# Performance work log

Hardware: AMD Instinct MI355X
Metric: run time of the kernel (lower is better)

The kernel has to match this reference:

```python
import jax, jax.numpy as jnp
import numpy as np

H = 64  # rnn_size == input_size
CANVAS = 25


def _init_params(key, vocab_size):
    ks = jax.random.split(key, 14)
    s = 0.05
    p = {}
    p['embed'] = jax.random.normal(ks[0], (vocab_size + 1, H), jnp.float32) * s
    p['W_ih'] = jax.random.normal(ks[1], (4 * H, H), jnp.float32) * s
    p['W_hh'] = jax.random.normal(ks[2], (4 * H, H), jnp.float32) * s
    p['b_ih'] = jax.random.normal(ks[3], (4 * H,), jnp.float32) * s
    p['b_hh'] = jax.random.normal(ks[4], (4 * H,), jnp.float32) * s
    p['Wc'] = jax.random.normal(ks[5], (3, H), jnp.float32) * s
    p['bc'] = jax.random.normal(ks[6], (3,), jnp.float32) * s
    p['Ws'] = jax.random.normal(ks[7], (3, H), jnp.float32) * s
    p['bs'] = jax.random.normal(ks[8], (3,), jnp.float32) * s
    p['Wo'] = jax.random.normal(ks[9], (2, H), jnp.float32) * s
    p['bo'] = jax.random.normal(ks[10], (2,), jnp.float32) * s
    p['Wr1'] = jax.random.normal(ks[11], (32, H + 1 + 4), jnp.float32) * s
    p['br1'] = jnp.zeros((32,), jnp.float32)
    p['Wr2'] = jax.random.normal(ks[12], (1, 32), jnp.float32) * s
    p['br2'] = jnp.zeros((1,), jnp.float32)
    return p


def setup_inputs() -> dict:
    key = jax.random.key(0)
    k1, k2, k3, k4, k5 = jax.random.split(key, 5)
    B, T, V = 4096, 128, 32000
    inp = {
        'inst': jax.random.randint(k1, (B, T), 0, V, dtype=jnp.int64)
        if jax.config.jax_enable_x64 else jax.random.randint(k1, (B, T), 0, V, dtype=jnp.int32),
        'prev_canvas': jax.random.normal(k2, (B, CANVAS, 4), jnp.float32),
        'ref_obj': jax.random.normal(k3, (B, 4), jnp.float32),
        'target_obj': jax.random.normal(k4, (B, 4), jnp.float32),
    }
    inp.update(_init_params(k5, V))
    return inp


def _encode(inst, embed, W_ih, W_hh, b_ih, b_hh):
    # inst: [B, T] -> h: [B, H] via sequential LSTMCell
    xs = embed[inst]                       # [B, T, H]
    xs = jnp.swapaxes(xs, 0, 1)            # [T, B, H]
    B = inst.shape[0]
    h0 = jnp.zeros((B, H), xs.dtype)
    c0 = jnp.zeros((B, H), xs.dtype)

    def step(carry, x):
        h, c = carry
        gates = x @ W_ih.T + b_ih + h @ W_hh.T + b_hh   # [B, 4H]
        i, f, g, o = jnp.split(gates, 4, axis=-1)
        i, f, o = jax.nn.sigmoid(i), jax.nn.sigmoid(f), jax.nn.sigmoid(o)
        c = f * c + i * jnp.tanh(g)
        h = o * jnp.tanh(c)
        return (h, c), None

    (h, _), _ = jax.lax.scan(step, (h0, c0), xs)
    return h


def _act_tag(inst):
    # 1.0 if last token with value >= 1 equals 9, else 0.0
    T = inst.shape[1]
    mask = inst >= 1                                   # [B, T]
    last_pos = T - 1 - jnp.argmax(mask[:, ::-1], axis=1)
    last_val = jnp.take_along_axis(inst, last_pos[:, None], axis=1)[:, 0]
    tag = jnp.where((last_val == 9) & mask.any(axis=1), 1.0, 0.0)
    return tag.astype(jnp.float32)


def reference(inst, prev_canvas, ref_obj, target_obj, embed, W_ih, W_hh, b_ih, b_hh,
              Wc, bc, Ws, bs, Wo, bo, Wr1, br1, Wr2, br2):
    h = _encode(inst, embed, W_ih, W_hh, b_ih, b_hh)           # [B, H]
    tag = _act_tag(inst)                                       # [B]
    inst2 = jnp.concatenate([h, tag[:, None]], axis=1)         # [B, H+1]
    inst2 = jnp.broadcast_to(inst2[:, None, :], (h.shape[0], CANVAS, H + 1))
    feat = jnp.concatenate([inst2, prev_canvas], axis=2)       # [B, 25, 69]
    hid = jax.nn.relu(jnp.einsum('bnf,of->bno', feat, Wr1) + br1)
    score = (jnp.einsum('bno,ro->bnr', hid, Wr2) + br2)[..., 0]  # [B, 25]
    weight = jax.nn.softmax(score, axis=1)
    ref_pred = jnp.einsum('bn,bnd->bd', weight, prev_canvas)   # [B, 4]
    offset = jnp.clip(h @ Wo.T + bo, -1.0, 1.0)                # hardtanh, [B, 2]
    color_out = jax.nn.log_softmax(h @ Wc.T + bc, axis=1)      # [B, 3]
    shape_out = jax.nn.log_softmax(h @ Ws.T + bs, axis=1)      # [B, 3]
    row_out = ref_pred[:, 2] + offset[:, 0]
    col_out = ref_pred[:, 3] + offset[:, 1]
    return (color_out, shape_out, row_out, col_out)
```

## Files before the change

kernel.cpp:

```cpp
#include <hip/hip_runtime.h>
#include <hip/hip_bf16.h>

#define HH 64
#define TT 128
#define BT 16

typedef __attribute__((ext_vector_type(8))) short bf16x8;
typedef __attribute__((ext_vector_type(4))) float f32x4;

__device__ __forceinline__ unsigned short f2bf(float f) {
  union { float f; unsigned u; } v; v.f = f;
  return (unsigned short)((v.u + 0x7FFFu + ((v.u >> 16) & 1u)) >> 16);
}
__device__ __forceinline__ float sigm(float x) {
  return __builtin_amdgcn_rcpf(1.f + __builtin_amdgcn_exp2f(-1.44269504f * x));
}
__device__ __forceinline__ float tanh_(float x) {
  x = fminf(fmaxf(x, -15.f), 15.f);
  float e = __builtin_amdgcn_exp2f(2.88539008f * x);
  return (e - 1.f) * __builtin_amdgcn_rcpf(e + 1.f);
}
__device__ __forceinline__ float wred64(float v) {
#pragma unroll
  for (int s = 32; s; s >>= 1) v += __shfl_xor(v, s);
  return v;
}

__global__ void convert_embed(const float* __restrict__ src,
                              unsigned short* __restrict__ dst, int n) {
  int base = (blockIdx.x * 256 + threadIdx.x) * 4;
  if (base + 4 <= n) {
    float4 v = *(const float4*)(src + base);
    ushort4 r;
    r.x = f2bf(v.x); r.y = f2bf(v.y); r.z = f2bf(v.z); r.w = f2bf(v.w);
    *(ushort4*)(dst + base) = r;
  } else {
    for (int k = base; k < n; k++) dst[k] = f2bf(src[k]);
  }
}

#define MFMA(acc, a, b) acc = __builtin_amdgcn_mfma_f32_16x16x32_bf16(a, b, acc, 0, 0, 0)

__global__ __launch_bounds__(256, 1) void lstm_k(
    const int* __restrict__ inst, const unsigned short* __restrict__ ebf,
    const float* __restrict__ Wih, const float* __restrict__ Whh,
    const float* __restrict__ bih, const float* __restrict__ bhh,
    float* __restrict__ hbuf)
{
  __shared__ int tokT[TT * BT];
  __shared__ unsigned short hsh[2 * BT * HH];

  const int tid  = threadIdx.x;
  const int lane = tid & 63;
  const int w    = tid >> 6;
  const int fr   = lane & 15;
  const int fg   = lane >> 4;
  const int b0   = blockIdx.x * BT;
  const int jcol = w * 16 + fr;

  for (int i = tid; i < BT * TT; i += 256)
    tokT[(i & (TT - 1)) * BT + (i >> 7)] = inst[b0 * TT + i];
  for (int i = tid; i < BT * HH; i += 256) hsh[i] = 0;

  bf16x8 wih[4][2], whh[4][2];
  float bias[4];
#pragma unroll
  for (int q = 0; q < 4; q++) {
    const int n = (w + q * 4) * 16 + fr;
    bias[q] = bih[n] + bhh[n];
#pragma unroll
    for (int kt = 0; kt < 2; kt++) {
      const float* pa = Wih + n * 64 + kt * 32 + fg * 8;
      const float* pb = Whh + n * 64 + kt * 32 + fg * 8;
      bf16x8 fa, fb;
#pragma unroll
      for (int j = 0; j < 8; j++) { fa[j] = (short)f2bf(pa[j]); fb[j] = (short)f2bf(pb[j]); }
      wih[q][kt] = fa; whh[q][kt] = fb;
    }
  }

  __syncthreads();

  bf16x8 xa0, xa1;
  {
    const int tk = tokT[0 * BT + fr];
    const unsigned short* p = ebf + tk * 64 + fg * 8;
    xa0 = *(const bf16x8*)p;
    xa1 = *(const bf16x8*)(p + 32);
  }

  float cst[4] = {0.f, 0.f, 0.f, 0.f};
  float hkeep[4] = {0.f, 0.f, 0.f, 0.f};

  for (int t = 0; t < TT; t++) {
    bf16x8 xn0 = xa0, xn1 = xa1;
    if (t + 1 < TT) {
      const int tk = tokT[(t + 1) * BT + fr];
      const unsigned short* p = ebf + tk * 64 + fg * 8;
      xn0 = *(const bf16x8*)p;
      xn1 = *(const bf16x8*)(p + 32);
    }

    const char* hb = (const char*)hsh + (t & 1) * (BT * HH * 2);
    const int sx = (fr & 7) << 4;
    bf16x8 ha0 = *(const bf16x8*)(hb + ((fr * 128 + fg * 16) ^ sx));
    bf16x8 ha1 = *(const bf16x8*)(hb + ((fr * 128 + 64 + fg * 16) ^ sx));

    f32x4 D0 = {0.f,0.f,0.f,0.f}, D1 = {0.f,0.f,0.f,0.f},
          D2 = {0.f,0.f,0.f,0.f}, D3 = {0.f,0.f,0.f,0.f};
    MFMA(D0, xa0, wih[0][0]); MFMA(D0, xa1, wih[0][1]);
    MFMA(D1, xa0, wih[1][0]); MFMA(D1, xa1, wih[1][1]);
    MFMA(D2, xa0, wih[2][0]); MFMA(D2, xa1, wih[2][1]);
    MFMA(D3, xa0, wih[3][0]); MFMA(D3, xa1, wih[3][1]);
    MFMA(D0, ha0, whh[0][0]); MFMA(D0, ha1, whh[0][1]);
    MFMA(D1, ha0, whh[1][0]); MFMA(D1, ha1, whh[1][1]);
    MFMA(D2, ha0, whh[2][0]); MFMA(D2, ha1, whh[2][1]);
    MFMA(D3, ha0, whh[3][0]); MFMA(D3, ha1, whh[3][1]);

    char* hwb = (char*)hsh + ((t + 1) & 1) * (BT * HH * 2);
#pragma unroll
    for (int r = 0; r < 4; r++) {
      const float gi = sigm(D0[r] + bias[0]);
      const float gf = sigm(D1[r] + bias[1]);
      const float gg = tanh_(D2[r] + bias[2]);
      const float go = sigm(D3[r] + bias[3]);
      const float cn = gf * cst[r] + gi * gg;
      cst[r] = cn;
      const float hn = go * tanh_(cn);
      hkeep[r] = hn;
      const int m = fg * 4 + r;
      *(unsigned short*)(hwb + ((m * 128 + 2 * jcol) ^ ((m & 7) << 4))) = f2bf(hn);
    }
    __syncthreads();
    xa0 = xn0; xa1 = xn1;
  }

#pragma unroll
  for (int r = 0; r < 4; r++) {
    const int m = fg * 4 + r;
    hbuf[(size_t)(b0 + m) * 64 + jcol] = hkeep[r];
  }
}

__global__ __launch_bounds__(256, 2) void head_k(
    const int* __restrict__ inst, const float* __restrict__ canvas,
    const float* __restrict__ hbuf,
    const float* __restrict__ Wc, const float* __restrict__ bc,
    const float* __restrict__ Ws, const float* __restrict__ bs,
    const float* __restrict__ Wo, const float* __restrict__ bo,
    const float* __restrict__ Wr1, const float* __restrict__ br1,
    const float* __restrict__ Wr2, const float* __restrict__ br2,
    float* __restrict__ out, int B)
{
  __shared__ float Wr1_s[32 * 69];
  __shared__ float h_s[4][64];
  __shared__ float cv_s[4][100];
  __shared__ float sc_s[4][25];

  const int tid = threadIdx.x, lane = tid & 63, w = tid >> 6;
  const int b = blockIdx.x * 4 + w;

  for (int i = tid; i < 32 * 69; i += 256) Wr1_s[i] = Wr1[i];
  const float hj = hbuf[(size_t)b * 64 + lane];
  h_s[w][lane] = hj;
  for (int idx = lane; idx < 100; idx += 64) cv_s[w][idx] = canvas[(size_t)b * 100 + idx];

  const int t1 = inst[(size_t)b * TT + lane];
  const int t2 = inst[(size_t)b * TT + 64 + lane];
  int key = -1;
  if (t1 >= 1) key = (lane << 16) | t1;
  if (t2 >= 1) key = ((64 + lane) << 16) | t2;
#pragma unroll
  for (int s = 32; s; s >>= 1) key = max(key, __shfl_xor(key, s));
  const float tag = (key >= 0 && (key & 0xFFFF) == 9) ? 1.f : 0.f;

  __syncthreads();

  const int o = lane & 31, half = lane >> 5;
  float base = br1[o] + Wr1_s[o * 69 + 64] * tag;
  for (int f = 0; f < 64; f++) base += Wr1_s[o * 69 + f] * h_s[w][f];
  const float wr2o = Wr2[o];
  const int n0 = half ? 13 : 0, n1 = half ? 25 : 13;
  for (int n = n0; n < n1; n++) {
    float acc = base;
#pragma unroll
    for (int d = 0; d < 4; d++) acc += Wr1_s[o * 69 + 65 + d] * cv_s[w][n * 4 + d];
    float p = wr2o * fmaxf(acc, 0.f);
#pragma unroll
    for (int s = 16; s; s >>= 1) p += __shfl_xor(p, s, 32);
    if (o == 0) sc_s[w][n] = p + br2[0];
  }
  __syncthreads();

  float mx = -1e30f;
  for (int n = 0; n < 25; n++) mx = fmaxf(mx, sc_s[w][n]);
  float sum = 0.f, rp2 = 0.f, rp3 = 0.f;
  for (int n = 0; n < 25; n++) {
    float e = __expf(sc_s[w][n] - mx);
    sum += e;
    rp2 += e * cv_s[w][n * 4 + 2];
    rp3 += e * cv_s[w][n * 4 + 3];
  }
  const float inv = 1.f / sum;

  float c0 = wred64(hj * Wc[lane]),      c1 = wred64(hj * Wc[64 + lane]),  c2 = wred64(hj * Wc[128 + lane]);
  float s0 = wred64(hj * Ws[lane]),      s1 = wred64(hj * Ws[64 + lane]),  s2 = wred64(hj * Ws[128 + lane]);
  float o0 = wred64(hj * Wo[lane]),      o1 = wred64(hj * Wo[64 + lane]);
  c0 += bc[0]; c1 += bc[1]; c2 += bc[2];
  s0 += bs[0]; s1 += bs[1]; s2 += bs[2];
  o0 = fminf(fmaxf(o0 + bo[0], -1.f), 1.f);
  o1 = fminf(fmaxf(o1 + bo[1], -1.f), 1.f);

  const float cm = fmaxf(c0, fmaxf(c1, c2));
  const float cl = cm + __logf(__expf(c0 - cm) + __expf(c1 - cm) + __expf(c2 - cm));
  const float smx = fmaxf(s0, fmaxf(s1, s2));
  const float sl = smx + __logf(__expf(s0 - smx) + __expf(s1 - smx) + __expf(s2 - smx));

  if (lane == 0) {
    out[b * 3 + 0] = c0 - cl; out[b * 3 + 1] = c1 - cl; out[b * 3 + 2] = c2 - cl;
    float* shp = out + (size_t)3 * B;
    shp[b * 3 + 0] = s0 - sl; shp[b * 3 + 1] = s1 - sl; shp[b * 3 + 2] = s2 - sl;
    out[(size_t)6 * B + b] = rp2 * inv + o0;
    out[(size_t)7 * B + b] = rp3 * inv + o1;
  }
}

extern "C" void kernel_launch(void* const* d_in, const int* in_sizes, int n_in,
                              void* d_out, int out_size, void* d_ws, size_t ws_size,
                              hipStream_t stream) {
  const int*   inst   = (const int*)  d_in[0];
  const float* canvas = (const float*)d_in[1];
  const float* embed  = (const float*)d_in[4];
  const float* Wih    = (const float*)d_in[5];
  const float* Whh    = (const float*)d_in[6];
  const float* bih    = (const float*)d_in[7];
  const float* bhh    = (const float*)d_in[8];
  const float* Wc     = (const float*)d_in[9];
  const float* bc     = (const float*)d_in[10];
  const float* Ws_    = (const float*)d_in[11];
  const float* bs     = (const float*)d_in[12];
  const float* Wo     = (const float*)d_in[13];
  const float* bo     = (const float*)d_in[14];
  const float* Wr1    = (const float*)d_in[15];
  const float* br1    = (const float*)d_in[16];
  const float* Wr2    = (const float*)d_in[17];
  const float* br2    = (const float*)d_in[18];

  const int B  = in_sizes[0] / TT;
  const int NE = in_sizes[4];

  unsigned short* ebf = (unsigned short*)d_ws;
  size_t ebytes = ((size_t)NE * 2 + 255) / 256 * 256;
  float* hbuf = (float*)((char*)d_ws + ebytes);

  convert_embed<<<(NE / 4 + 255) / 256, 256, 0, stream>>>(embed, ebf, NE);
  lstm_k<<<B / BT, 256, 0, stream>>>(inst, ebf, Wih, Whh, bih, bhh, hbuf);
  head_k<<<B / 4, 256, 0, stream>>>(inst, canvas, hbuf, Wc, bc, Ws_, bs, Wo, bo,
                                    Wr1, br1, Wr2, br2, (float*)d_out, B);
}
```

Measured before the change: 108.6 us.

## Fuse head into LSTM kernel and split gate work across 8 waves

The LSTM kernel now runs 512 threads per block. Half the waves compute the input and cell gates, and the other half compute the forget and output gates plus the cell update, exchanging results through shared memory with two barriers per step. The input projection for the next step is computed off the critical path after the first barrier. The head computation is fused into the same kernel, reading h from shared memory, which removes the hbuf round trip and one kernel launch. The cost is a second barrier per timestep and extra shared-memory traffic in the recurrent loop.

```diff
diff --git a/kernel.cpp b/kernel.cpp
--- a/kernel.cpp
+++ b/kernel.cpp
@@ -12,17 +12,15 @@
   union { float f; unsigned u; } v; v.f = f;
   return (unsigned short)((v.u + 0x7FFFu + ((v.u >> 16) & 1u)) >> 16);
 }
-__device__ __forceinline__ float sigm(float x) {
-  return __builtin_amdgcn_rcpf(1.f + __builtin_amdgcn_exp2f(-1.44269504f * x));
-}
-__device__ __forceinline__ float tanh_(float x) {
-  x = fminf(fmaxf(x, -15.f), 15.f);
-  float e = __builtin_amdgcn_exp2f(2.88539008f * x);
-  return (e - 1.f) * __builtin_amdgcn_rcpf(e + 1.f);
-}
-__device__ __forceinline__ float wred64(float v) {
-#pragma unroll
-  for (int s = 32; s; s >>= 1) v += __shfl_xor(v, s);
+__device__ __forceinline__ float rcp_(float x) { return __builtin_amdgcn_rcpf(x); }
+__device__ __forceinline__ float exp2_(float x) { return __builtin_amdgcn_exp2f(x); }
+
+#define L2E 1.44269504f
+#define L2E2 2.88539008f
+
+__device__ __forceinline__ float red32(float v) {
+#pragma unroll
+  for (int s = 16; s; s >>= 1) v += __shfl_xor(v, s, 32);
   return v;
 }
 
@@ -41,110 +39,11 @@
 
 #define MFMA(acc, a, b) acc = __builtin_amdgcn_mfma_f32_16x16x32_bf16(a, b, acc, 0, 0, 0)
 
-__global__ __launch_bounds__(256, 1) void lstm_k(
+__global__ __launch_bounds__(512, 1) void lstm_k(
     const int* __restrict__ inst, const unsigned short* __restrict__ ebf,
     const float* __restrict__ Wih, const float* __restrict__ Whh,
     const float* __restrict__ bih, const float* __restrict__ bhh,
-    float* __restrict__ hbuf)
-{
-  __shared__ int tokT[TT * BT];
-  __shared__ unsigned short hsh[2 * BT * HH];
-
-  const int tid  = threadIdx.x;
-  const int lane = tid & 63;
-  const int w    = tid >> 6;
-  const int fr   = lane & 15;
-  const int fg   = lane >> 4;
-  const int b0   = blockIdx.x * BT;
-  const int jcol = w * 16 + fr;
-
-  for (int i = tid; i < BT * TT; i += 256)
-    tokT[(i & (TT - 1)) * BT + (i >> 7)] = inst[b0 * TT + i];
-  for (int i = tid; i < BT * HH; i += 256) hsh[i] = 0;
-
-  bf16x8 wih[4][2], whh[4][2];
-  float bias[4];
-#pragma unroll
-  for (int q = 0; q < 4; q++) {
-    const int n = (w + q * 4) * 16 + fr;
-    bias[q] = bih[n] + bhh[n];
-#pragma unroll
-    for (int kt = 0; kt < 2; kt++) {
-      const float* pa = Wih + n * 64 + kt * 32 + fg * 8;
-      const float* pb = Whh + n * 64 + kt * 32 + fg * 8;
-      bf16x8 fa, fb;
-#pragma unroll
-      for (int j = 0; j < 8; j++) { fa[j] = (short)f2bf(pa[j]); fb[j] = (short)f2bf(pb[j]); }
-      wih[q][kt] = fa; whh[q][kt] = fb;
-    }
-  }
-
-  __syncthreads();
-
-  bf16x8 xa0, xa1;
-  {
-    const int tk = tokT[0 * BT + fr];
-    const unsigned short* p = ebf + tk * 64 + fg * 8;
-    xa0 = *(const bf16x8*)p;
-    xa1 = *(const bf16x8*)(p + 32);
-  }
-
-  float cst[4] = {0.f, 0.f, 0.f, 0.f};
-  float hkeep[4] = {0.f, 0.f, 0.f, 0.f};
-
-  for (int t = 0; t < TT; t++) {
-    bf16x8 xn0 = xa0, xn1 = xa1;
-    if (t + 1 < TT) {
-      const int tk = tokT[(t + 1) * BT + fr];
-      const unsigned short* p = ebf + tk * 64 + fg * 8;
-      xn0 = *(const bf16x8*)p;
-      xn1 = *(const bf16x8*)(p + 32);
-    }
-
-    const char* hb = (const char*)hsh + (t & 1) * (BT * HH * 2);
-    const int sx = (fr & 7) << 4;
-    bf16x8 ha0 = *(const bf16x8*)(hb + ((fr * 128 + fg * 16) ^ sx));
-    bf16x8 ha1 = *(const bf16x8*)(hb + ((fr * 128 + 64 + fg * 16) ^ sx));
-
-    f32x4 D0 = {0.f,0.f,0.f,0.f}, D1 = {0.f,0.f,0.f,0.f},
-          D2 = {0.f,0.f,0.f,0.f}, D3 = {0.f,0.f,0.f,0.f};
-    MFMA(D0, xa0, wih[0][0]); MFMA(D0, xa1, wih[0][1]);
-    MFMA(D1, xa0, wih[1][0]); MFMA(D1, xa1, wih[1][1]);
-    MFMA(D2, xa0, wih[2][0]); MFMA(D2, xa1, wih[2][1]);
-    MFMA(D3, xa0, wih[3][0]); MFMA(D3, xa1, wih[3][1]);
-    MFMA(D0, ha0, whh[0][0]); MFMA(D0, ha1, whh[0][1]);
-    MFMA(D1, ha0, whh[1][0]); MFMA(D1, ha1, whh[1][1]);
-    MFMA(D2, ha0, whh[2][0]); MFMA(D2, ha1, whh[2][1]);
-    MFMA(D3, ha0, whh[3][0]); MFMA(D3, ha1, whh[3][1]);
-
-    char* hwb = (char*)hsh + ((t + 1) & 1) * (BT * HH * 2);
-#pragma unroll
-    for (int r = 0; r < 4; r++) {
-      const float gi = sigm(D0[r] + bias[0]);
-      const float gf = sigm(D1[r] + bias[1]);
-      const float gg = tanh_(D2[r] + bias[2]);
-      const float go = sigm(D3[r] + bias[3]);
-      const float cn = gf * cst[r] + gi * gg;
-      cst[r] = cn;
-      const float hn = go * tanh_(cn);
-      hkeep[r] = hn;
-      const int m = fg * 4 + r;
-      *(unsigned short*)(hwb + ((m * 128 + 2 * jcol) ^ ((m & 7) << 4))) = f2bf(hn);
-    }
-    __syncthreads();
-    xa0 = xn0; xa1 = xn1;
-  }
-
-#pragma unroll
-  for (int r = 0; r < 4; r++) {
-    const int m = fg * 4 + r;
-    hbuf[(size_t)(b0 + m) * 64 + jcol] = hkeep[r];
-  }
-}
-
-__global__ __launch_bounds__(256, 2) void head_k(
-    const int* __restrict__ inst, const float* __restrict__ canvas,
-    const float* __restrict__ hbuf,
+    const float* __restrict__ canvas,
     const float* __restrict__ Wc, const float* __restrict__ bc,
     const float* __restrict__ Ws, const float* __restrict__ bs,
     const float* __restrict__ Wo, const float* __restrict__ bo,
@@ -152,76 +51,189 @@
     const float* __restrict__ Wr2, const float* __restrict__ br2,
     float* __restrict__ out, int B)
 {
+  __shared__ int tokT[TT * BT];
+  __shared__ unsigned short hsh[2 * BT * HH];
+  __shared__ float a_s[16][66];
   __shared__ float Wr1_s[32 * 69];
-  __shared__ float h_s[4][64];
-  __shared__ float cv_s[4][100];
-  __shared__ float sc_s[4][25];
-
-  const int tid = threadIdx.x, lane = tid & 63, w = tid >> 6;
-  const int b = blockIdx.x * 4 + w;
-
-  for (int i = tid; i < 32 * 69; i += 256) Wr1_s[i] = Wr1[i];
-  const float hj = hbuf[(size_t)b * 64 + lane];
-  h_s[w][lane] = hj;
-  for (int idx = lane; idx < 100; idx += 64) cv_s[w][idx] = canvas[(size_t)b * 100 + idx];
-
-  const int t1 = inst[(size_t)b * TT + lane];
-  const int t2 = inst[(size_t)b * TT + 64 + lane];
+
+  const int tid  = threadIdx.x;
+  const int lane = tid & 63;
+  const int w    = tid >> 6;
+  const int wid  = w & 3;
+  const int hi   = w >> 2;
+  const int fr   = lane & 15;
+  const int fg   = lane >> 4;
+  const int b0   = blockIdx.x * BT;
+  const int jcol = wid * 16 + fr;
+  const int n0   = hi * 64 + jcol;
+  const int n1   = n0 + 128;
+
+  for (int i = tid; i < BT * TT; i += 512)
+    tokT[(i & (TT - 1)) * BT + (i >> 7)] = inst[b0 * TT + i];
+  for (int i = tid; i < BT * HH; i += 512) hsh[i] = 0;
+  for (int i = tid; i < 32 * 69; i += 512) Wr1_s[i] = Wr1[i];
+
+  bf16x8 wt[2][2][2];
+  float nb0, sb1;
+#pragma unroll
+  for (int tile = 0; tile < 2; tile++) {
+    const int n = tile ? n1 : n0;
+#pragma unroll
+    for (int kt = 0; kt < 2; kt++) {
+      const float* pa = Wih + n * 64 + kt * 32 + fg * 8;
+      const float* pb = Whh + n * 64 + kt * 32 + fg * 8;
+      bf16x8 fa, fb;
+#pragma unroll
+      for (int j = 0; j < 8; j++) { fa[j] = (short)f2bf(pa[j]); fb[j] = (short)f2bf(pb[j]); }
+      wt[tile][kt][0] = fa; wt[tile][kt][1] = fb;
+    }
+  }
+  nb0 = -L2E * (bih[n0] + bhh[n0]);
+  sb1 = (hi ? -L2E : L2E2) * (bih[n1] + bhh[n1]);
+
+  bf16x8 xa0, xa1;
+  {
+    const int tk = tokT[0 * BT + fr];
+    const unsigned short* p = ebf + tk * 64 + fg * 8;
+    xa0 = *(const bf16x8*)p; xa1 = *(const bf16x8*)(p + 32);
+  }
+  f32x4 Dx0 = {0.f,0.f,0.f,0.f}, Dx1 = {0.f,0.f,0.f,0.f};
+  MFMA(Dx0, xa0, wt[0][0][0]); MFMA(Dx0, xa1, wt[0][1][0]);
+  MFMA(Dx1, xa0, wt[1][0][0]); MFMA(Dx1, xa1, wt[1][1][0]);
+  {
+    const int tk = tokT[1 * BT + fr];
+    const unsigned short* p = ebf + tk * 64 + fg * 8;
+    xa0 = *(const bf16x8*)p; xa1 = *(const bf16x8*)(p + 32);
+  }
+
+  float cst[4] = {0.f,0.f,0.f,0.f};
+  float pf[4], po[4];
+
+  __syncthreads();
+
+  for (int t = 0; t < TT; t++) {
+    const char* hb = (const char*)hsh + (t & 1) * (BT * HH * 2);
+    const int sx = (fr & 7) << 4;
+    bf16x8 ha0 = *(const bf16x8*)(hb + ((fr * 128 + fg * 16) ^ sx));
+    bf16x8 ha1 = *(const bf16x8*)(hb + ((fr * 128 + 64 + fg * 16) ^ sx));
+
+    f32x4 D0 = Dx0, D1 = Dx1;
+    MFMA(D0, ha0, wt[0][0][1]); MFMA(D0, ha1, wt[0][1][1]);
+    MFMA(D1, ha0, wt[1][0][1]); MFMA(D1, ha1, wt[1][1][1]);
+
+    if (hi == 0) {
+#pragma unroll
+      for (int r = 0; r < 4; r++) {
+        const int m = fg * 4 + r;
+        const float gi = rcp_(1.f + exp2_(fmaf(D0[r], -L2E, nb0)));
+        const float e  = exp2_(fmaf(D1[r], L2E2, sb1));
+        const float tg = (e - 1.f) * rcp_(e + 1.f);
+        a_s[m][jcol] = gi * tg;
+      }
+    } else {
+#pragma unroll
+      for (int r = 0; r < 4; r++) {
+        pf[r] = rcp_(1.f + exp2_(fmaf(D0[r], -L2E, nb0)));
+        po[r] = rcp_(1.f + exp2_(fmaf(D1[r], -L2E, sb1)));
+      }
+    }
+    __syncthreads();
+
+    if (t + 1 < TT) {
+      f32x4 nx0 = {0.f,0.f,0.f,0.f}, nx1 = {0.f,0.f,0.f,0.f};
+      MFMA(nx0, xa0, wt[0][0][0]); MFMA(nx0, xa1, wt[0][1][0]);
+      MFMA(nx1, xa0, wt[1][0][0]); MFMA(nx1, xa1, wt[1][1][0]);
+      Dx0 = nx0; Dx1 = nx1;
+      if (t + 2 < TT) {
+        const int tk = tokT[(t + 2) * BT + fr];
+        const unsigned short* p = ebf + tk * 64 + fg * 8;
+        xa0 = *(const bf16x8*)p; xa1 = *(const bf16x8*)(p + 32);
+      }
+    }
+    if (hi == 1) {
+      char* hwb = (char*)hsh + ((t + 1) & 1) * (BT * HH * 2);
+#pragma unroll
+      for (int r = 0; r < 4; r++) {
+        const int m = fg * 4 + r;
+        const float a = a_s[m][jcol];
+        const float c = fmaf(pf[r], cst[r], a);
+        cst[r] = c;
+        const float e  = exp2_(L2E2 * fminf(c, 15.f));
+        const float th = (e - 1.f) * rcp_(e + 1.f);
+        const float hn = po[r] * th;
+        *(unsigned short*)(hwb + ((m * 128 + 2 * jcol) ^ ((m & 7) << 4))) = f2bf(hn);
+        if (t == TT - 1) a_s[m][jcol] = hn;
+      }
+    }
+    __syncthreads();
+  }
+
+  const int m  = (w << 1) + (lane >> 5);
+  const int o  = lane & 31;
+  const int gb = b0 + m;
+
   int key = -1;
-  if (t1 >= 1) key = (lane << 16) | t1;
-  if (t2 >= 1) key = ((64 + lane) << 16) | t2;
-#pragma unroll
-  for (int s = 32; s; s >>= 1) key = max(key, __shfl_xor(key, s));
+#pragma unroll
+  for (int q = 0; q < 4; q++) {
+    const int t = o + q * 32;
+    const int tk = tokT[t * BT + m];
+    if (tk >= 1) key = max(key, (t << 16) | tk);
+  }
+#pragma unroll
+  for (int s = 16; s; s >>= 1) key = max(key, __shfl_xor(key, s, 32));
   const float tag = (key >= 0 && (key & 0xFFFF) == 9) ? 1.f : 0.f;
 
-  __syncthreads();
-
-  const int o = lane & 31, half = lane >> 5;
   float base = br1[o] + Wr1_s[o * 69 + 64] * tag;
-  for (int f = 0; f < 64; f++) base += Wr1_s[o * 69 + f] * h_s[w][f];
+  for (int f = 0; f < 64; f++) base += Wr1_s[o * 69 + f] * a_s[m][f];
   const float wr2o = Wr2[o];
-  const int n0 = half ? 13 : 0, n1 = half ? 25 : 13;
-  for (int n = n0; n < n1; n++) {
+  const float* cv = canvas + (size_t)gb * 100;
+
+  float sc[25];
+  float mx = -1e30f;
+#pragma unroll
+  for (int n = 0; n < 25; n++) {
     float acc = base;
 #pragma unroll
-    for (int d = 0; d < 4; d++) acc += Wr1_s[o * 69 + 65 + d] * cv_s[w][n * 4 + d];
+    for (int d = 0; d < 4; d++) acc += Wr1_s[o * 69 + 65 + d] * cv[n * 4 + d];
     float p = wr2o * fmaxf(acc, 0.f);
 #pragma unroll
     for (int s = 16; s; s >>= 1) p += __shfl_xor(p, s, 32);
-    if (o == 0) sc_s[w][n] = p + br2[0];
-  }
-  __syncthreads();
-
-  float mx = -1e30f;
-  for (int n = 0; n < 25; n++) mx = fmaxf(mx, sc_s[w][n]);
+    sc[n] = p + br2[0];
+    mx = fmaxf(mx, sc[n]);
+  }
   float sum = 0.f, rp2 = 0.f, rp3 = 0.f;
+#pragma unroll
   for (int n = 0; n < 25; n++) {
-    float e = __expf(sc_s[w][n] - mx);
+    const float e = __expf(sc[n] - mx);
     sum += e;
-    rp2 += e * cv_s[w][n * 4 + 2];
-    rp3 += e * cv_s[w][n * 4 + 3];
+    rp2 += e * cv[n * 4 + 2];
+    rp3 += e * cv[n * 4 + 3];
   }
   const float inv = 1.f / sum;
 
-  float c0 = wred64(hj * Wc[lane]),      c1 = wred64(hj * Wc[64 + lane]),  c2 = wred64(hj * Wc[128 + lane]);
-  float s0 = wred64(hj * Ws[lane]),      s1 = wred64(hj * Ws[64 + lane]),  s2 = wred64(hj * Ws[128 + lane]);
-  float o0 = wred64(hj * Wo[lane]),      o1 = wred64(hj * Wo[64 + lane]);
-  c0 += bc[0]; c1 += bc[1]; c2 += bc[2];
-  s0 += bs[0]; s1 += bs[1]; s2 += bs[2];
-  o0 = fminf(fmaxf(o0 + bo[0], -1.f), 1.f);
-  o1 = fminf(fmaxf(o1 + bo[1], -1.f), 1.f);
+  const float h0 = a_s[m][o], h1 = a_s[m][o + 32];
+  float c0 = red32(h0 * Wc[o]       + h1 * Wc[32 + o]) + bc[0];
+  float c1 = red32(h0 * Wc[64 + o]  + h1 * Wc[96 + o]) + bc[1];
+  float c2 = red32(h0 * Wc[128 + o] + h1 * Wc[160 + o]) + bc[2];
+  float s0 = red32(h0 * Ws[o]       + h1 * Ws[32 + o]) + bs[0];
+  float s1 = red32(h0 * Ws[64 + o]  + h1 * Ws[96 + o]) + bs[1];
+  float s2 = red32(h0 * Ws[128 + o] + h1 * Ws[160 + o]) + bs[2];
+  float o0 = red32(h0 * Wo[o]       + h1 * Wo[32 + o]) + bo[0];
+  float o1 = red32(h0 * Wo[64 + o]  + h1 * Wo[96 + o]) + bo[1];
+  o0 = fminf(fmaxf(o0, -1.f), 1.f);
+  o1 = fminf(fmaxf(o1, -1.f), 1.f);
 
   const float cm = fmaxf(c0, fmaxf(c1, c2));
   const float cl = cm + __logf(__expf(c0 - cm) + __expf(c1 - cm) + __expf(c2 - cm));
-  const float smx = fmaxf(s0, fmaxf(s1, s2));
-  const float sl = smx + __logf(__expf(s0 - smx) + __expf(s1 - smx) + __expf(s2 - smx));
-
-  if (lane == 0) {
-    out[b * 3 + 0] = c0 - cl; out[b * 3 + 1] = c1 - cl; out[b * 3 + 2] = c2 - cl;
+  const float sm = fmaxf(s0, fmaxf(s1, s2));
+  const float sl = sm + __logf(__expf(s0 - sm) + __expf(s1 - sm) + __expf(s2 - sm));
+
+  if (o == 0) {
+    out[gb * 3 + 0] = c0 - cl; out[gb * 3 + 1] = c1 - cl; out[gb * 3 + 2] = c2 - cl;
     float* shp = out + (size_t)3 * B;
-    shp[b * 3 + 0] = s0 - sl; shp[b * 3 + 1] = s1 - sl; shp[b * 3 + 2] = s2 - sl;
-    out[(size_t)6 * B + b] = rp2 * inv + o0;
-    out[(size_t)7 * B + b] = rp3 * inv + o1;
+    shp[gb * 3 + 0] = s0 - sl; shp[gb * 3 + 1] = s1 - sl; shp[gb * 3 + 2] = s2 - sl;
+    out[(size_t)6 * B + gb] = rp2 * inv + o0;
+    out[(size_t)7 * B + gb] = rp3 * inv + o1;
   }
 }
 
@@ -250,11 +262,9 @@
   const int NE = in_sizes[4];
 
   unsigned short* ebf = (unsigned short*)d_ws;
-  size_t ebytes = ((size_t)NE * 2 + 255) / 256 * 256;
-  float* hbuf = (float*)((char*)d_ws + ebytes);
 
   convert_embed<<<(NE / 4 + 255) / 256, 256, 0, stream>>>(embed, ebf, NE);
-  lstm_k<<<B / BT, 256, 0, stream>>>(inst, ebf, Wih, Whh, bih, bhh, hbuf);
-  head_k<<<B / 4, 256, 0, stream>>>(inst, canvas, hbuf, Wc, bc, Ws_, bs, Wo, bo,
-                                    Wr1, br1, Wr2, br2, (float*)d_out, B);
-}
+  lstm_k<<<B / BT, 512, 0, stream>>>(inst, ebf, Wih, Whh, bih, bhh,
+                                     canvas, Wc, bc, Ws_, bs, Wo, bo,
+                                     Wr1, br1, Wr2, br2, (float*)d_out, B);
+}
```

Result: slower. 112.8 us (+3.8%).
